# Kernel tuning notes

Hardware: AMD Instinct MI355X
Metric: run time of the kernel (lower is better)

The kernel has to match this reference:

```python
import jax, jax.numpy as jnp
from jax import lax
import numpy as np

# 8-neighbor topology from the original module
TOPO = np.array([[0, 1], [1, 1], [1, 0], [1, -1], [0, -1], [-1, -1], [-1, 0], [-1, 1]])
EPS = 1e-5


def conv(x, w, stride=1, pad=0, groups=1):
    # NCHW / OIHW convolution, no bias (module uses bias=False everywhere)
    return lax.conv_general_dilated(
        x, w, (stride, stride), [(pad, pad), (pad, pad)],
        feature_group_count=groups,
        dimension_numbers=('NCHW', 'OIHW', 'NCHW'))


def bn(x, g, b):
    # training-mode BatchNorm2d (batch statistics, biased variance)
    m = jnp.mean(x, axis=(0, 2, 3), keepdims=True)
    v = jnp.var(x, axis=(0, 2, 3), keepdims=True)
    return g[None, :, None, None] * (x - m) * lax.rsqrt(v + EPS) + b[None, :, None, None]


def setup_inputs() -> dict:
    key = jax.random.key(0)
    ks = jax.random.split(key, 12)
    B, D, NC, H, W = 8, 6, 48, 256, 256
    s = 0.1
    w = lambda k, shape: jax.random.normal(k, shape, jnp.float32) * s
    return dict(
        x=jax.random.normal(ks[0], (B, D, H, W), jnp.float32),
        # compenv_conv: Conv(D->NC,1) BN tanh Conv(NC->1,1)
        ce_w1=w(ks[1], (NC, D, 1, 1)), ce_g=jnp.ones(NC), ce_b=jnp.zeros(NC),
        ce_w2=w(ks[2], (1, NC, 1, 1)),
        # merge_change_determinant: funnel(ConvT(10->NC,3) tanh Conv(NC->NC,3) tanh) BN tanh Conv(NC->1,2,s2) sigmoid
        # ConvT stride-1 k3 expressed as pad-2 conv with conv-equivalent kernel
        md_ct=w(ks[3], (NC, 10, 3, 3)), md_c1=w(ks[4], (NC, NC, 3, 3)),
        md_g=jnp.ones(NC), md_b=jnp.zeros(NC), md_c2=w(ks[5], (1, NC, 2, 2)),
        # cell_merge: Conv(D->NC,2,s2,g3) BN tanh funnel(ConvT(NC->NC,3,g3) tanh Conv(NC->D,3,g3) tanh)
        cm_w1=w(ks[6], (NC, D // 3, 2, 2)), cm_g=jnp.ones(NC), cm_b=jnp.zeros(NC),
        cm_ct=w(ks[7], (NC, NC // 3, 3, 3)), cm_c2=w(ks[8], (D, NC // 3, 3, 3)),
        # born: Conv(D->NC,1) BN tanh Conv(NC->D,1)
        bo_w1=w(ks[9], (NC, D, 1, 1)), bo_g=jnp.ones(NC), bo_b=jnp.zeros(NC),
        bo_w2=w(ks[10], (D, NC, 1, 1)),
    )


def reference(x, ce_w1, ce_g, ce_b, ce_w2, md_ct, md_c1, md_g, md_b, md_c2,
              cm_w1, cm_g, cm_b, cm_ct, cm_c2, bo_w1, bo_g, bo_b, bo_w2):
    # ---- compenv: per-direction roll + 1x1conv/BN/tanh/1x1conv (BN stats per direction, as in torch) ----
    env = []
    for k in range(8):
        t = jnp.roll(x, int(TOPO[k, 0]), axis=3)      # roll_right along W
        t = jnp.roll(t, int(-TOPO[k, 1]), axis=2)     # roll_down along H
        h = jnp.tanh(bn(conv(t, ce_w1), ce_g, ce_b))
        env.append(conv(h, ce_w2))                    # [B,1,H,W]
    ENV = jnp.concatenate(env, axis=1)                # [B,8,H,W]

    # ---- merge change determinant ----
    te = jnp.concatenate([x[:, :2], ENV], axis=1)     # [B,10,H,W]
    h = jnp.tanh(conv(te, md_ct, pad=2))              # ConvT k3 s1 == pad-2 conv -> [B,NC,H+2,W+2]
    h = jnp.tanh(conv(h, md_c1))                      # -> [B,NC,H,W]
    h = jnp.tanh(bn(h, md_g, md_b))
    CHANGE = jax.nn.sigmoid(conv(h, md_c2, stride=2))  # [B,1,H/2,W/2]

    # ---- cell merge ----
    h = jnp.tanh(bn(conv(x, cm_w1, stride=2, groups=3), cm_g, cm_b))  # [B,NC,H/2,W/2]
    h = jnp.tanh(conv(h, cm_ct, pad=2, groups=3))
    xm = jnp.tanh(conv(h, cm_c2, groups=3))           # [B,D,H/2,W/2]

    # ---- born + blend ----
    born = conv(jnp.tanh(bn(conv(xm, bo_w1), bo_g, bo_b)), bo_w2)
    out = xm * (1.0 - CHANGE) + CHANGE * born
    out = jnp.concatenate([jax.nn.sigmoid(out[:, :3]), out[:, 3:]], axis=1)
    return out
```

## Files before the change

kernel.cpp:

```cpp
#include <hip/hip_runtime.h>
#include <stdint.h>

typedef unsigned short ushort_t;

#define B8  8
#define D6  6
#define NC  48
#define HH  256
#define WW  256
#define HWp 65536
#define H2  128
#define HW2 16384

__device__ __constant__ int c_T0[8] = {0,1,1,1,0,-1,-1,-1};
__device__ __constant__ int c_T1[8] = {1,1,0,-1,-1,-1,0,1};

__device__ inline float bf2f(ushort_t u){ union{unsigned int i; float f;} w; w.i = ((unsigned int)u)<<16; return w.f; }
__device__ inline ushort_t f2bf(float f){ union{float f; unsigned int i;} w; w.f=f; unsigned int xx=w.i;
  return (ushort_t)((xx + 0x7fffu + ((xx>>16)&1u)) >> 16); }
__device__ inline float tanhf_(float x){ float e=__expf(2.f*x); return 1.f - 2.f/(e+1.f); }
__device__ inline float sigm_(float x){ return 1.f/(1.f+__expf(-x)); }
__device__ inline float ldg_(const void* p, size_t i, int isbf){
  return isbf ? bf2f(((const ushort_t*)p)[i]) : ((const float*)p)[i];
}

typedef short short8 __attribute__((ext_vector_type(8)));
typedef float f4 __attribute__((ext_vector_type(4)));
typedef ushort_t us4 __attribute__((ext_vector_type(4)));
typedef ushort_t us8 __attribute__((ext_vector_type(8)));
union AB { short8 s; us4 h[2]; us8 u; };

__global__ __launch_bounds__(256) void k_detect(const ushort_t* x, float* flag){
  int t=threadIdx.x; int cnt=0;
  for(int i=t;i<4096;i+=256){
    ushort_t u=x[2*i];
    int e=(u>>7)&0xff;
    if(e>=100 && e<=150) cnt++;
  }
  for(int o=32;o;o>>=1) cnt+=__shfl_down(cnt,o,64);
  __shared__ int sh4[4];
  if((t&63)==0) sh4[t>>6]=cnt;
  __syncthreads();
  if(t==0){ int tot=sh4[0]+sh4[1]+sh4[2]+sh4[3]; flag[0] = (tot>=2048)?1.f:0.f; }
}

struct WC { const ushort_t* src[10]; int off[10]; int n[10]; };

__global__ __launch_bounds__(256) void k_wcvt(WC wc, float* dst, const float* dfl){
  int isbf = dfl[0]>0.5f;
  int t = blockIdx.y; int n = wc.n[t]; const ushort_t* s = wc.src[t]; float* d = dst + wc.off[t];
  for(int i = blockIdx.x*256 + threadIdx.x; i < n; i += gridDim.x*256)
    d[i] = isbf ? bf2f(s[i]) : ((const float*)s)[i];
}

__global__ __launch_bounds__(256) void k_wprep(const float* w2src, const float* w1src,
                                               ushort_t* wb2, ushort_t* wb1){
  int t = blockIdx.x*256+threadIdx.x;
  if(t<3456){
    int lane=t&63; int rest=t>>6;
    int ks=rest&1; int g=rest>>1; int tap=g%9; int nt=g/9;
    int oc=nt*16+(lane&15); int icb=ks*32+((lane>>4)*8);
    #pragma unroll
    for(int j=0;j<8;j++){
      int ic=icb+j;
      float v = (ic<48) ? w2src[(oc*48+ic)*9+tap] : 0.f;
      wb2[(size_t)t*8+j]=f2bf(v);
    }
  } else if(t<5184){
    int tt=t-3456; int lane=tt&63; int g=tt>>6; int tap=g%9; int nt=g/9;
    int oc=nt*16+(lane&15); int icb=(lane>>4)*8;
    #pragma unroll
    for(int j=0;j<8;j++){
      int ic=icb+j;
      float v = (ic<10) ? w1src[(oc*10+ic)*9+tap] : 0.f;
      wb1[(size_t)tt*8+j]=f2bf(v);
    }
  }
}

__global__ __launch_bounds__(256) void k_mom(const void* src, const float* dfl, int isbfc,
                                             int sh, int npix, float* out){
  int isbf = dfl ? (dfl[0]>0.5f) : isbfc;
  float vals[27];
  #pragma unroll
  for(int i=0;i<27;i++) vals[i]=0.f;
  int stride = gridDim.x*256;
  int msk = (1<<sh)-1;
  for(int p = blockIdx.x*256+threadIdx.x; p < npix; p += stride){
    int b = p >> sh; int hw = p & msk;
    float v[6];
    #pragma unroll
    for(int d=0; d<6; d++){
      size_t idx = (((size_t)(b*6+d))<<sh) + hw;
      v[d] = ldg_(src, idx, isbf);
    }
    int q=6;
    #pragma unroll
    for(int d=0;d<6;d++){
      vals[d]+=v[d];
      #pragma unroll
      for(int e=d;e<6;e++){ vals[q] += v[d]*v[e]; q++; }
    }
  }
  __shared__ float red[4][27];
  int wid=threadIdx.x>>6, lane=threadIdx.x&63;
  #pragma unroll
  for(int i=0;i<27;i++){
    float v=vals[i];
    for(int o=32;o;o>>=1) v+=__shfl_down(v,o,64);
    if(lane==0) red[wid][i]=v;
  }
  __syncthreads();
  if(threadIdx.x<27)
    atomicAdd(&out[threadIdx.x],
      red[0][threadIdx.x]+red[1][threadIdx.x]+red[2][threadIdx.x]+red[3][threadIdx.x]);
}

__global__ __launch_bounds__(64) void k_msb(const float* mom, const float* W1,
      const void* g, const void* b, const float* dfl, float invN, float* scale, float* bias){
  int c = threadIdx.x; if(c>=NC) return;
  int isbf = dfl[0]>0.5f;
  const int st[6]={0,6,11,15,18,20};
  float wr[6];
  #pragma unroll
  for(int d=0;d<6;d++) wr[d]=W1[c*6+d];
  float mean=0.f;
  #pragma unroll
  for(int d=0;d<6;d++) mean += wr[d]*mom[d];
  mean *= invN;
  float e2=0.f;
  #pragma unroll
  for(int d=0;d<6;d++){
    #pragma unroll
    for(int e=d;e<6;e++){
      float mm = mom[6 + st[d] + (e-d)];
      e2 += wr[d]*wr[e]*((e==d)?1.f:2.f)*mm;
    }
  }
  e2 *= invN;
  float var = e2 - mean*mean;
  float sc = ldg_(g,c,isbf) * rsqrtf(var + 1e-5f);
  scale[c]=sc; bias[c]= ldg_(b,c,isbf) - sc*mean;
}

__global__ __launch_bounds__(256) void k_env(const void* x, const float* dfl,
      const float* w1, const float* w2, const float* sc, const float* bi, float* e){
  int isbf = dfl[0]>0.5f;
  int p = blockIdx.x*256+threadIdx.x;
  int b = p >> 16; int hw = p & 65535;
  float v[6];
  #pragma unroll
  for(int d=0; d<6; d++) v[d]=ldg_(x,(size_t)(b*6+d)*HWp + hw, isbf);
  float acc=0.f;
  for(int c=0;c<NC;c++){
    float y=0.f;
    #pragma unroll
    for(int d=0;d<6;d++) y += w1[c*6+d]*v[d];
    acc += w2[c]*tanhf_(sc[c]*y + bi[c]);
  }
  e[(size_t)b*HWp + hw]=acc;
}

__global__ __launch_bounds__(256) void k_h1m(const void* x, const float* dfl, const float* e,
      const ushort_t* wb1, ushort_t* h1cl){
  __shared__ __attribute__((aligned(16))) ushort_t tile[324*24];
  int isbf = dfl[0]>0.5f;
  int b = blockIdx.y;
  int ti = blockIdx.x/17, tj = blockIdx.x%17;
  int i0 = ti*16, j0 = tj*16;
  {
    us8 z;
    #pragma unroll
    for(int j=0;j<8;j++) z[j]=0;
    us8* tp=(us8*)tile;
    for(int idx=threadIdx.x; idx<972; idx+=256) tp[idx]=z;
  }
  __syncthreads();
  for(int idx=threadIdx.x; idx<3240; idx+=256){
    int pix = idx/10, ic = idx-pix*10;
    int r = pix/18, c = pix-r*18;
    int gy = i0-2+r, gx = j0-2+c;
    float v = 0.f;
    if(gy>=0 && gy<HH && gx>=0 && gx<WW){
      if(ic<2) v = ldg_(x, ((size_t)(b*6+ic)*HH + gy)*WW + gx, isbf);
      else { int k=ic-2;
        int yy=(gy + c_T1[k]) & 255; int xx=(gx - c_T0[k]) & 255;
        v = e[((size_t)b*HH + yy)*WW + xx]; }
    }
    tile[pix*24+ic]=f2bf(v);
  }
  __syncthreads();
  int lane = threadIdx.x&63, w = threadIdx.x>>6;
  int n = lane&15, quad = lane>>4;
  int qoff = (quad<2) ? quad*8 : 16;
  f4 acc[4][3];
  #pragma unroll
  for(int a=0;a<4;a++)
    #pragma unroll
    for(int c=0;c<3;c++) acc[a][c]=(f4){0.f,0.f,0.f,0.f};
  for(int tap=0; tap<9; tap++){
    int ki=tap/3, kj=tap%3;
    AB Bf[3];
    #pragma unroll
    for(int nt=0;nt<3;nt++) Bf[nt].u = *(const us8*)&wb1[((size_t)((nt*9+tap)*64+lane))*8];
    #pragma unroll
    for(int yy=0; yy<4; yy++){
      int y = w*4 + yy;
      AB a; a.u = *(const us8*)&tile[((y+ki)*18 + n + kj)*24 + qoff];
      #pragma unroll
      for(int nt=0;nt<3;nt++)
        acc[yy][nt] = __builtin_amdgcn_mfma_f32_16x16x32_bf16(a.s, Bf[nt].s, acc[yy][nt], 0,0,0);
    }
  }
  #pragma unroll
  for(int yy=0;yy<4;yy++){
    int Y = i0 + w*4 + yy;
    if(Y>=258) continue;
    #pragma unroll
    for(int nt=0;nt<3;nt++){
      int oc = nt*16 + n;
      #pragma unroll
      for(int r=0;r<4;r++){
        int X = j0 + quad*4 + r;
        if(X<258)
          h1cl[(((size_t)b*258 + Y)*258 + X)*48 + oc] = f2bf(tanhf_(acc[yy][nt][r]));
      }
    }
  }
}

__global__ __launch_bounds__(256) void k_h2m(const ushort_t* h1cl, const ushort_t* wb2,
      ushort_t* h2h, float* stats){
  __shared__ float red[4][3][16][2];
  int b = blockIdx.y;
  int ti = blockIdx.x>>4, tj = blockIdx.x&15;
  int i0 = ti*16, j0 = tj*16;
  int lane = threadIdx.x&63, w = threadIdx.x>>6;
  int n = lane&15, quad = lane>>4;
  f4 acc[4][3];
  #pragma unroll
  for(int a=0;a<4;a++)
    #pragma unroll
    for(int c=0;c<3;c++) acc[a][c]=(f4){0.f,0.f,0.f,0.f};
  for(int tap=0; tap<9; tap++){
    int ki=tap/3, kj=tap%3;
    AB Bf[3][2];
    #pragma unroll
    for(int nt=0;nt<3;nt++)
      #pragma unroll
      for(int ks=0;ks<2;ks++)
        Bf[nt][ks].u = *(const us8*)&wb2[((size_t)(((nt*9+tap)*2+ks)*64+lane))*8];
    #pragma unroll
    for(int yy=0; yy<4; yy++){
      int Y = i0 + w*4 + yy;
      const ushort_t* ap = &h1cl[(((size_t)b*258 + Y+ki)*258 + (j0+n+kj))*48 + quad*8];
      AB a0, a1;
      a0.u = *(const us8*)ap;
      a1.u = *(const us8*)(ap+32);
      #pragma unroll
      for(int nt=0;nt<3;nt++){
        acc[yy][nt] = __builtin_amdgcn_mfma_f32_16x16x32_bf16(a0.s, Bf[nt][0].s, acc[yy][nt], 0,0,0);
        acc[yy][nt] = __builtin_amdgcn_mfma_f32_16x16x32_bf16(a1.s, Bf[nt][1].s, acc[yy][nt], 0,0,0);
      }
    }
  }
  float s[3]={0.f,0.f,0.f}, q[3]={0.f,0.f,0.f};
  #pragma unroll
  for(int yy=0;yy<4;yy++){
    int Y = i0 + w*4 + yy;
    #pragma unroll
    for(int nt=0;nt<3;nt++){
      int oc = nt*16 + n;
      size_t base = ((size_t)(b*NC+oc)*HH + Y)*WW + j0 + quad*4;
      us4 u;
      #pragma unroll
      for(int r=0;r<4;r++){
        float v=tanhf_(acc[yy][nt][r]);
        u[r]=f2bf(v);
        float vb=bf2f(u[r]);
        s[nt]+=vb; q[nt]+=vb*vb;
      }
      *(us4*)&h2h[base] = u;
    }
  }
  #pragma unroll
  for(int nt=0;nt<3;nt++){
    s[nt]+=__shfl_xor(s[nt],16,64); s[nt]+=__shfl_xor(s[nt],32,64);
    q[nt]+=__shfl_xor(q[nt],16,64); q[nt]+=__shfl_xor(q[nt],32,64);
  }
  if(quad==0){
    #pragma unroll
    for(int nt=0;nt<3;nt++){ red[w][nt][n][0]=s[nt]; red[w][nt][n][1]=q[nt]; }
  }
  __syncthreads();
  if(threadIdx.x<48){
    int oc=threadIdx.x; int nt=oc>>4, nn=oc&15;
    float S=red[0][nt][nn][0]+red[1][nt][nn][0]+red[2][nt][nn][0]+red[3][nt][nn][0];
    float Q=red[0][nt][nn][1]+red[1][nt][nn][1]+red[2][nt][nn][1]+red[3][nt][nn][1];
    atomicAdd(&stats[2*oc],S); atomicAdd(&stats[2*oc+1],Q);
  }
}

__global__ __launch_bounds__(256) void k_cstat(const float* srcf, const ushort_t* srch, int isbf,
      int C, int HWn, int Bn, int S, float* stats){
  int c = blockIdx.x % C; int s = blockIdx.x / C;
  float sum=0.f, sq=0.f;
  for(int b=0;b<Bn;b++){
    size_t base=((size_t)b*C+c)*HWn;
    for(int i=s*256+threadIdx.x; i<HWn; i+=S*256){
      float v = isbf ? bf2f(srch[base+i]) : srcf[base+i];
      sum+=v; sq+=v*v;
    }
  }
  for(int o=32;o;o>>=1){ sum+=__shfl_down(sum,o,64); sq+=__shfl_down(sq,o,64); }
  __shared__ float ls[4], lq[4];
  int wid=threadIdx.x>>6;
  if((threadIdx.x&63)==0){ ls[wid]=sum; lq[wid]=sq; }
  __syncthreads();
  if(threadIdx.x==0){
    atomicAdd(&stats[2*c],   ls[0]+ls[1]+ls[2]+ls[3]);
    atomicAdd(&stats[2*c+1], lq[0]+lq[1]+lq[2]+lq[3]);
  }
}

__global__ __launch_bounds__(64) void k_csb(const float* stats, const void* g, const void* b,
      const float* dfl, float invN, float* scale, float* bias){
  int c=threadIdx.x; if(c>=NC) return;
  int isbf = dfl[0]>0.5f;
  float mean=stats[2*c]*invN; float var=stats[2*c+1]*invN - mean*mean;
  float s=ldg_(g,c,isbf)*rsqrtf(var+1e-5f);
  scale[c]=s; bias[c]=ldg_(b,c,isbf)-s*mean;
}

__global__ __launch_bounds__(256) void k_change(const ushort_t* h2h,
      const float* wc2, const float* sc, const float* bi, float* CH){
  int p=blockIdx.x*256+threadIdx.x;
  int b=p>>14; int rem=p&16383; int i=rem>>7; int j=rem&127;
  float acc=0.f;
  for(int ic=0;ic<NC;ic++){
    size_t base=((size_t)(b*NC+ic)*HH + 2*i)*WW + 2*j;
    float s=sc[ic], t=bi[ic];
    #pragma unroll
    for(int ki=0;ki<2;ki++)
      #pragma unroll
      for(int kj=0;kj<2;kj++){
        float v= bf2f(h2h[base+(size_t)ki*WW+kj]);
        acc += tanhf_(s*v+t)*wc2[ic*4+ki*2+kj];
      }
  }
  CH[p]=sigm_(acc);
}

__global__ __launch_bounds__(256) void k_cm1(const void* x, const float* dfl, const float* w, float* t1){
  int isbf = dfl[0]>0.5f;
  int p=blockIdx.x*256+threadIdx.x;
  int b=p>>14; int rem=p&16383; int i=rem>>7; int j=rem&127;
  float v[6][2][2];
  #pragma unroll
  for(int d=0;d<6;d++)
    #pragma unroll
    for(int ki=0;ki<2;ki++)
      #pragma unroll
      for(int kj=0;kj<2;kj++)
        v[d][ki][kj]=ldg_(x, ((size_t)(b*6+d)*HH + 2*i+ki)*WW + 2*j+kj, isbf);
  for(int oc=0;oc<NC;oc++){
    int g=oc>>4;
    float a=0.f;
    #pragma unroll
    for(int icl=0;icl<2;icl++)
      #pragma unroll
      for(int ki=0;ki<2;ki++)
        #pragma unroll
        for(int kj=0;kj<2;kj++)
          a += v[2*g+icl][ki][kj]*w[((oc*2+icl)*2+ki)*2+kj];
    t1[((size_t)(b*NC+oc)*HW2) + rem]=a;
  }
}

__global__ __launch_bounds__(256) void k_cm2(const float* t1, const float* sc, const float* bi,
        const float* wct, float* t2){
  __shared__ float as[16][20][21];
  int b=blockIdx.y, g=blockIdx.z;
  int ti=blockIdx.x/9, tj=blockIdx.x%9;
  int i0=ti*16, j0=tj*16;
  int ty=threadIdx.x>>4, tx=threadIdx.x&15;
  for(int idx=threadIdx.x; idx<6400; idx+=256){
    int i=idx/400; int rem=idx-i*400; int r=rem/20; int cc=rem-r*20;
    int cg=g*16+i;
    int y=i0-2+r, xx=j0-2+cc;
    float v=0.f;
    if(y>=0 && y<H2 && xx>=0 && xx<H2)
      v = tanhf_(sc[cg]*t1[((size_t)(b*NC+cg)*H2 + y)*H2 + xx] + bi[cg]);
    as[i][r][cc]=v;
  }
  __syncthreads();
  float acc[16];
  #pragma unroll
  for(int o=0;o<16;o++) acc[o]=0.f;
  for(int i=0;i<16;i++){
    float p[3][3];
    #pragma unroll
    for(int ki=0;ki<3;ki++)
      #pragma unroll
      for(int kj=0;kj<3;kj++) p[ki][kj]=as[i][ty+ki][tx+kj];
    #pragma unroll
    for(int o=0;o<16;o++){
      const float* wp=&wct[((size_t)(g*16+o)*16+i)*9];
      float a=0.f;
      #pragma unroll
      for(int q=0;q<9;q++) a += p[q/3][q%3]*wp[q];
      acc[o]+=a;
    }
  }
  int ii=i0+ty, jj=j0+tx;
  if(ii<130 && jj<130){
    #pragma unroll
    for(int o=0;o<16;o++)
      t2[((size_t)(b*NC+g*16+o)*130 + ii)*130 + jj]=tanhf_(acc[o]);
  }
}

__global__ __launch_bounds__(256) void k_cm3(const float* t2, const float* w, float* xm){
  __shared__ float ts[16][18][20];
  int b=blockIdx.y, g=blockIdx.z;
  int ti=blockIdx.x>>3, tj=blockIdx.x&7;
  int i0=ti*16, j0=tj*16;
  int ty=threadIdx.x>>4, tx=threadIdx.x&15;
  for(int idx=threadIdx.x; idx<16*18*18; idx+=256){
    int i=idx/324; int rem=idx-i*324; int r=rem/18; int cc=rem-r*18;
    int cg=g*16+i;
    ts[i][r][cc]=t2[((size_t)(b*NC+cg)*130 + i0+r)*130 + j0+cc];
  }
  __syncthreads();
  float acc[2]={0.f,0.f};
  for(int icl=0;icl<16;icl++){
    float p[3][3];
    #pragma unroll
    for(int ki=0;ki<3;ki++)
      #pragma unroll
      for(int kj=0;kj<3;kj++) p[ki][kj]=ts[icl][ty+ki][tx+kj];
    #pragma unroll
    for(int ol=0;ol<2;ol++){
      int oc=2*g+ol;
      const float* wp=&w[((size_t)oc*16+icl)*9];
      float a=0.f;
      #pragma unroll
      for(int q=0;q<9;q++) a += p[q/3][q%3]*wp[q];
      acc[ol]+=a;
    }
  }
  int ii=i0+ty, jj=j0+tx;
  #pragma unroll
  for(int ol=0;ol<2;ol++)
    xm[((size_t)(b*6+2*g+ol)*H2 + ii)*H2 + jj]=tanhf_(acc[ol]);
}

__global__ __launch_bounds__(256) void k_final(const float* xm, const float* CH, const float* w1,
      const float* w2, const float* sc, const float* bi, const float* dfl, void* outp){
  int isbf = dfl[0]>0.5f;
  int p=blockIdx.x*256+threadIdx.x;
  int b=p>>14; int rem=p&16383;
  float v[6];
  #pragma unroll
  for(int d=0;d<6;d++) v[d]=xm[((size_t)(b*6+d)*HW2)+rem];
  float born[6]={0.f,0.f,0.f,0.f,0.f,0.f};
  for(int c=0;c<NC;c++){
    float y=0.f;
    #pragma unroll
    for(int d=0;d<6;d++) y+=w1[c*6+d]*v[d];
    float a=tanhf_(sc[c]*y+bi[c]);
    #pragma unroll
    for(int d=0;d<6;d++) born[d]+=w2[d*NC+c]*a;
  }
  float C=CH[p];
  #pragma unroll
  for(int d=0;d<6;d++){
    float o=v[d]*(1.f-C)+C*born[d];
    if(d<3) o=sigm_(o);
    size_t id=((size_t)(b*6+d)*HW2)+rem;
    if(isbf) ((ushort_t*)outp)[id]=f2bf(o); else ((float*)outp)[id]=o;
  }
}

extern "C" void kernel_launch(void* const* d_in, const int* in_sizes, int n_in,
                              void* d_out, int out_size, void* d_ws, size_t ws_size,
                              hipStream_t stream){
  (void)in_sizes; (void)n_in; (void)out_size; (void)ws_size;
  const ushort_t* x    = (const ushort_t*)d_in[0];
  const ushort_t* cew1 = (const ushort_t*)d_in[1];
  const void*     ceg  = d_in[2];
  const void*     ceb  = d_in[3];
  const ushort_t* cew2 = (const ushort_t*)d_in[4];
  const ushort_t* mdct = (const ushort_t*)d_in[5];
  const ushort_t* mdc1 = (const ushort_t*)d_in[6];
  const void*     mdg  = d_in[7];
  const void*     mdb  = d_in[8];
  const ushort_t* mdc2 = (const ushort_t*)d_in[9];
  const ushort_t* cmw1 = (const ushort_t*)d_in[10];
  const void*     cmg  = d_in[11];
  const void*     cmb  = d_in[12];
  const ushort_t* cmct = (const ushort_t*)d_in[13];
  const ushort_t* cmc2 = (const ushort_t*)d_in[14];
  const ushort_t* bow1 = (const ushort_t*)d_in[15];
  const void*     bog  = d_in[16];
  const void*     bob  = d_in[17];
  const ushort_t* bow2 = (const ushort_t*)d_in[18];
  float* ws = (float*)d_ws;

  const long OW_mdct=0, OW_mdc1=4320, OW_cew1=25056, OW_cew2=25344, OW_mdc2=25392,
             OW_cmw1=25584, OW_cmct=25968, OW_cmc2=32880, OW_bow1=33744, OW_bow2=34032;
  const long OFF_STATS=34320;
  const long ST_xmom=OFF_STATS+0,  ST_cesc=OFF_STATS+64,  ST_cebi=OFF_STATS+112,
             ST_h2  =OFF_STATS+160, ST_mdsc=OFF_STATS+256, ST_mdbi=OFF_STATS+304,
             ST_t1  =OFF_STATS+352, ST_cmsc=OFF_STATS+448, ST_cmbi=OFF_STATS+496,
             ST_xmm =OFF_STATS+544, ST_bosc=OFF_STATS+608, ST_bobi=OFF_STATS+656,
             ST_FLAG=OFF_STATS+960;
  const long OFF_WB2 = OFF_STATS + 1024;
  const long OFF_WB1 = OFF_WB2 + 13824;
  const long OFF_E   = OFF_WB1 + 6912;
  const long OFF_H2  = OFF_E + 524288L;
  const long OFF_D   = OFF_H2 + 12582912L;
  const long OFF_T1=OFF_D, OFF_T2=OFF_D+6291456L, OFF_XM=OFF_D+12781056L, OFF_CH=OFF_D+13567488L;

  ushort_t* h1cl = (ushort_t*)(ws + OFF_D);
  ushort_t* h2h  = (ushort_t*)(ws + OFF_H2);
  ushort_t* wb2  = (ushort_t*)(ws + OFF_WB2);
  ushort_t* wb1  = (ushort_t*)(ws + OFF_WB1);
  const float* dfl = ws + ST_FLAG;

  (void)hipMemsetAsync(ws + OFF_STATS, 0, 1024*sizeof(float), stream);
  hipLaunchKernelGGL(k_detect, dim3(1), 256, 0, stream, x, ws+ST_FLAG);

  WC wc;
  const ushort_t* srcs[10] = {mdct,mdc1,cew1,cew2,mdc2,cmw1,cmct,cmc2,bow1,bow2};
  const int offs[10] = {(int)OW_mdct,(int)OW_mdc1,(int)OW_cew1,(int)OW_cew2,(int)OW_mdc2,
                        (int)OW_cmw1,(int)OW_cmct,(int)OW_cmc2,(int)OW_bow1,(int)OW_bow2};
  const int cnts[10] = {4320,20736,288,48,192,384,6912,864,288,288};
  for(int i=0;i<10;i++){ wc.src[i]=srcs[i]; wc.off[i]=offs[i]; wc.n[i]=cnts[i]; }
  hipLaunchKernelGGL(k_wcvt, dim3(81,10), 256, 0, stream, wc, ws, dfl);
  hipLaunchKernelGGL(k_wprep, dim3(21), 256, 0, stream, ws+OW_mdc1, ws+OW_mdct, wb2, wb1);

  hipLaunchKernelGGL(k_mom, dim3(256), 256, 0, stream, (const void*)x, dfl, 0, 16, B8*HWp, ws+ST_xmom);
  hipLaunchKernelGGL(k_msb, dim3(1), 64, 0, stream, ws+ST_xmom, ws+OW_cew1, ceg, ceb, dfl,
                     1.f/(float)(B8*HWp), ws+ST_cesc, ws+ST_cebi);
  hipLaunchKernelGGL(k_env, dim3(2048), 256, 0, stream, (const void*)x, dfl, ws+OW_cew1, ws+OW_cew2,
                     ws+ST_cesc, ws+ST_cebi, ws+OFF_E);

  hipLaunchKernelGGL(k_h1m, dim3(289,8), 256, 0, stream, (const void*)x, dfl, ws+OFF_E, wb1, h1cl);
  hipLaunchKernelGGL(k_h2m, dim3(256,8), 256, 0, stream, h1cl, wb2, h2h, ws+ST_h2);
  hipLaunchKernelGGL(k_csb, dim3(1), 64, 0, stream, ws+ST_h2, mdg, mdb, dfl, 1.f/(float)(B8*HWp),
                     ws+ST_mdsc, ws+ST_mdbi);
  hipLaunchKernelGGL(k_change, dim3(512), 256, 0, stream, h2h, ws+OW_mdc2,
                     ws+ST_mdsc, ws+ST_mdbi, ws+OFF_CH);

  hipLaunchKernelGGL(k_cm1, dim3(512), 256, 0, stream, (const void*)x, dfl, ws+OW_cmw1, ws+OFF_T1);
  hipLaunchKernelGGL(k_cstat, dim3(48*8), 256, 0, stream, ws+OFF_T1, (const ushort_t*)nullptr, 0,
                     NC, HW2, B8, 8, ws+ST_t1);
  hipLaunchKernelGGL(k_csb, dim3(1), 64, 0, stream, ws+ST_t1, cmg, cmb, dfl, 1.f/(float)(B8*HW2),
                     ws+ST_cmsc, ws+ST_cmbi);
  hipLaunchKernelGGL(k_cm2, dim3(81,8,3), 256, 0, stream, ws+OFF_T1, ws+ST_cmsc, ws+ST_cmbi,
                     ws+OW_cmct, ws+OFF_T2);
  hipLaunchKernelGGL(k_cm3, dim3(64,8,3), 256, 0, stream, ws+OFF_T2, ws+OW_cmc2, ws+OFF_XM);

  hipLaunchKernelGGL(k_mom, dim3(128), 256, 0, stream, (const void*)(ws+OFF_XM), (const float*)nullptr, 0,
                     14, B8*HW2, ws+ST_xmm);
  hipLaunchKernelGGL(k_msb, dim3(1), 64, 0, stream, ws+ST_xmm, ws+OW_bow1, bog, bob, dfl,
                     1.f/(float)(B8*HW2), ws+ST_bosc, ws+ST_bobi);
  hipLaunchKernelGGL(k_final, dim3(512), 256, 0, stream, ws+OFF_XM, ws+OFF_CH, ws+OW_bow1,
                     ws+OW_bow2, ws+ST_bosc, ws+ST_bobi, dfl, d_out);
}
```

Before: 497.1 us.

## Stage h1 halo tile in LDS via async global_load_lds in k_h2m

k_h2m now copies each wave's 6x18x48 bf16 input halo into LDS with asynchronous global-to-LDS loads. The 3x3 conv's A fragments are then read from LDS instead of re-read from global memory for every tap, which removes repeated global traffic. The upper channel half for quads 2-3 now reads a zeroed LDS pad. The change also fully unrolls the tap loops in both conv kernels and adds a min-blocks-per-CU hint of 3. The cost is about 41KB of LDS per block, which may limit occupancy, plus register pressure from the unrolling.

```diff
diff --git a/kernel.cpp b/kernel.cpp
--- a/kernel.cpp
+++ b/kernel.cpp
@@ -198,6 +198,7 @@
   for(int a=0;a<4;a++)
     #pragma unroll
     for(int c=0;c<3;c++) acc[a][c]=(f4){0.f,0.f,0.f,0.f};
+  #pragma unroll
   for(int tap=0; tap<9; tap++){
     int ki=tap/3, kj=tap%3;
     AB Bf[3];
@@ -229,19 +230,38 @@
   }
 }
 
-__global__ __launch_bounds__(256) void k_h2m(const ushort_t* h1cl, const ushort_t* wb2,
+__global__ __launch_bounds__(256,3) void k_h2m(const ushort_t* h1cl, const ushort_t* wb2,
       ushort_t* h2h, float* stats){
+  __shared__ __attribute__((aligned(16))) ushort_t tile[20800];
   __shared__ float red[4][3][16][2];
   int b = blockIdx.y;
   int ti = blockIdx.x>>4, tj = blockIdx.x&15;
   int i0 = ti*16, j0 = tj*16;
   int lane = threadIdx.x&63, w = threadIdx.x>>6;
+  ushort_t* wtile = &tile[w*5200];
+  int r0 = i0 + w*4;
+  #pragma unroll
+  for(int it=0; it<11; it++){
+    int chunk = it*64 + lane;
+    if(chunk < 648){
+      int cpix = chunk/6, cq = chunk - cpix*6;
+      int rr = cpix/18, cc = cpix - rr*18;
+      const ushort_t* src = &h1cl[(((size_t)b*258 + r0+rr)*258 + (j0+cc))*48 + cq*8];
+      __builtin_amdgcn_global_load_lds(
+          (const __attribute__((address_space(1))) unsigned int*)src,
+          (__attribute__((address_space(3))) unsigned int*)(wtile + it*512),
+          16, 0, 0);
+    }
+  }
+  if(lane<16) wtile[5184+lane]=0;
+  __builtin_amdgcn_s_waitcnt(0x0F70);
   int n = lane&15, quad = lane>>4;
   f4 acc[4][3];
   #pragma unroll
   for(int a=0;a<4;a++)
     #pragma unroll
     for(int c=0;c<3;c++) acc[a][c]=(f4){0.f,0.f,0.f,0.f};
+  #pragma unroll
   for(int tap=0; tap<9; tap++){
     int ki=tap/3, kj=tap%3;
     AB Bf[3][2];
@@ -252,11 +272,11 @@
         Bf[nt][ks].u = *(const us8*)&wb2[((size_t)(((nt*9+tap)*2+ks)*64+lane))*8];
     #pragma unroll
     for(int yy=0; yy<4; yy++){
-      int Y = i0 + w*4 + yy;
-      const ushort_t* ap = &h1cl[(((size_t)b*258 + Y+ki)*258 + (j0+n+kj))*48 + quad*8];
+      int pix = (yy+ki)*18 + n + kj;
       AB a0, a1;
-      a0.u = *(const us8*)ap;
-      a1.u = *(const us8*)(ap+32);
+      a0.u = *(const us8*)(wtile + pix*48 + quad*8);
+      a1.u = (quad<2) ? *(const us8*)(wtile + pix*48 + 32 + quad*8)
+                      : *(const us8*)(wtile + 5184);
       #pragma unroll
       for(int nt=0;nt<3;nt++){
         acc[yy][nt] = __builtin_amdgcn_mfma_f32_16x16x32_bf16(a0.s, Bf[nt][0].s, acc[yy][nt], 0,0,0);
@@ -267,7 +287,7 @@
   float s[3]={0.f,0.f,0.f}, q[3]={0.f,0.f,0.f};
   #pragma unroll
   for(int yy=0;yy<4;yy++){
-    int Y = i0 + w*4 + yy;
+    int Y = r0 + yy;
     #pragma unroll
     for(int nt=0;nt<3;nt++){
       int oc = nt*16 + n;
```

Result: no change. 489.9 us (-1.5%).

## Fuse merge-determinant conv pair in shared memory; store cell-merge intermediate as bf16

Applied to the files above, without the earlier changes.

Fuses the two 3x3 convolutions of the merge-change branch into one kernel. Each block computes its 18x18 halo of the first conv's output (tanh applied) into LDS and feeds it straight to the second conv's MFMA loop, so the large channels-last h1 buffer is never written to or read back from global memory. The cost is recomputing the halo rows and columns and using much more LDS per block, which may lower occupancy (launch bounds now ask for 3 blocks). Separately, the cell-merge first-conv output t1 is stored as bf16 instead of fp32 to halve its traffic, at some precision cost before BN and tanh.

```diff
diff --git a/kernel.cpp b/kernel.cpp
--- a/kernel.cpp
+++ b/kernel.cpp
@@ -161,24 +161,29 @@
   e[(size_t)b*HWp + hw]=acc;
 }
 
-__global__ __launch_bounds__(256) void k_h1m(const void* x, const float* dfl, const float* e,
-      const ushort_t* wb1, ushort_t* h1cl){
-  __shared__ __attribute__((aligned(16))) ushort_t tile[324*24];
+__global__ __launch_bounds__(256,3) void k_md(const void* x, const float* dfl, const float* e,
+      const ushort_t* wb1, const ushort_t* wb2, ushort_t* h2h, float* stats){
+  __shared__ __attribute__((aligned(16))) ushort_t te[6400];
+  __shared__ __attribute__((aligned(16))) ushort_t h1t[18816];
+  __shared__ float red[4][3][16][2];
   int isbf = dfl[0]>0.5f;
   int b = blockIdx.y;
-  int ti = blockIdx.x/17, tj = blockIdx.x%17;
+  int ti = blockIdx.x>>4, tj = blockIdx.x&15;
   int i0 = ti*16, j0 = tj*16;
+  int lane = threadIdx.x&63, w = threadIdx.x>>6;
+  int n = lane&15, quad = lane>>4;
   {
     us8 z;
     #pragma unroll
     for(int j=0;j<8;j++) z[j]=0;
-    us8* tp=(us8*)tile;
-    for(int idx=threadIdx.x; idx<972; idx+=256) tp[idx]=z;
-  }
-  __syncthreads();
-  for(int idx=threadIdx.x; idx<3240; idx+=256){
+    us8* tp=(us8*)te;
+    for(int idx=threadIdx.x; idx<800; idx+=256) tp[idx]=z;
+    for(int idx=threadIdx.x; idx<336; idx+=256) *(us8*)&h1t[idx*56+48]=z;
+  }
+  __syncthreads();
+  for(int idx=threadIdx.x; idx<4000; idx+=256){
     int pix = idx/10, ic = idx-pix*10;
-    int r = pix/18, c = pix-r*18;
+    int r = pix/20, c = pix-r*20;
     int gy = i0-2+r, gx = j0-2+c;
     float v = 0.f;
     if(gy>=0 && gy<HH && gx>=0 && gx<WW){
@@ -187,61 +192,44 @@
         int yy=(gy + c_T1[k]) & 255; int xx=(gx - c_T0[k]) & 255;
         v = e[((size_t)b*HH + yy)*WW + xx]; }
     }
-    tile[pix*24+ic]=f2bf(v);
-  }
-  __syncthreads();
-  int lane = threadIdx.x&63, w = threadIdx.x>>6;
-  int n = lane&15, quad = lane>>4;
-  int qoff = (quad<2) ? quad*8 : 16;
+    te[pix*16+ic]=f2bf(v);
+  }
+  __syncthreads();
+  {
+    int qoff = (quad&1)*8;
+    for(int mt=w; mt<21; mt+=4){
+      int p = mt*16 + n;
+      int pr = p/18, pc = p-pr*18;
+      f4 hacc[3];
+      #pragma unroll
+      for(int nt=0;nt<3;nt++) hacc[nt]=(f4){0.f,0.f,0.f,0.f};
+      #pragma unroll
+      for(int tap=0; tap<9; tap++){
+        int ki=tap/3, kj=tap%3;
+        AB a; a.u = *(const us8*)&te[((pr+ki)*20 + pc+kj)*16 + qoff];
+        #pragma unroll
+        for(int nt=0;nt<3;nt++){
+          AB Bf; Bf.u = *(const us8*)&wb1[((size_t)((nt*9+tap)*64+lane))*8];
+          hacc[nt] = __builtin_amdgcn_mfma_f32_16x16x32_bf16(a.s, Bf.s, hacc[nt], 0,0,0);
+        }
+      }
+      int pd = mt*16 + quad*4;
+      #pragma unroll
+      for(int nt=0;nt<3;nt++){
+        #pragma unroll
+        for(int r=0;r<4;r++)
+          h1t[(pd+r)*56 + nt*16 + n] = f2bf(tanhf_(hacc[nt][r]));
+      }
+    }
+  }
+  __syncthreads();
   f4 acc[4][3];
   #pragma unroll
   for(int a=0;a<4;a++)
     #pragma unroll
     for(int c=0;c<3;c++) acc[a][c]=(f4){0.f,0.f,0.f,0.f};
-  for(int tap=0; tap<9; tap++){
-    int ki=tap/3, kj=tap%3;
-    AB Bf[3];
-    #pragma unroll
-    for(int nt=0;nt<3;nt++) Bf[nt].u = *(const us8*)&wb1[((size_t)((nt*9+tap)*64+lane))*8];
-    #pragma unroll
-    for(int yy=0; yy<4; yy++){
-      int y = w*4 + yy;
-      AB a; a.u = *(const us8*)&tile[((y+ki)*18 + n + kj)*24 + qoff];
-      #pragma unroll
-      for(int nt=0;nt<3;nt++)
-        acc[yy][nt] = __builtin_amdgcn_mfma_f32_16x16x32_bf16(a.s, Bf[nt].s, acc[yy][nt], 0,0,0);
-    }
-  }
-  #pragma unroll
-  for(int yy=0;yy<4;yy++){
-    int Y = i0 + w*4 + yy;
-    if(Y>=258) continue;
-    #pragma unroll
-    for(int nt=0;nt<3;nt++){
-      int oc = nt*16 + n;
-      #pragma unroll
-      for(int r=0;r<4;r++){
-        int X = j0 + quad*4 + r;
-        if(X<258)
-          h1cl[(((size_t)b*258 + Y)*258 + X)*48 + oc] = f2bf(tanhf_(acc[yy][nt][r]));
-      }
-    }
-  }
-}
-
-__global__ __launch_bounds__(256) void k_h2m(const ushort_t* h1cl, const ushort_t* wb2,
-      ushort_t* h2h, float* stats){
-  __shared__ float red[4][3][16][2];
-  int b = blockIdx.y;
-  int ti = blockIdx.x>>4, tj = blockIdx.x&15;
-  int i0 = ti*16, j0 = tj*16;
-  int lane = threadIdx.x&63, w = threadIdx.x>>6;
-  int n = lane&15, quad = lane>>4;
-  f4 acc[4][3];
-  #pragma unroll
-  for(int a=0;a<4;a++)
-    #pragma unroll
-    for(int c=0;c<3;c++) acc[a][c]=(f4){0.f,0.f,0.f,0.f};
+  int q1off = 32 + ((quad<2) ? quad*8 : 16);
+  #pragma unroll
   for(int tap=0; tap<9; tap++){
     int ki=tap/3, kj=tap%3;
     AB Bf[3][2];
@@ -252,11 +240,11 @@
         Bf[nt][ks].u = *(const us8*)&wb2[((size_t)(((nt*9+tap)*2+ks)*64+lane))*8];
     #pragma unroll
     for(int yy=0; yy<4; yy++){
-      int Y = i0 + w*4 + yy;
-      const ushort_t* ap = &h1cl[(((size_t)b*258 + Y+ki)*258 + (j0+n+kj))*48 + quad*8];
+      int y = w*4 + yy;
+      int base = ((y+ki)*18 + n + kj)*56;
       AB a0, a1;
-      a0.u = *(const us8*)ap;
-      a1.u = *(const us8*)(ap+32);
+      a0.u = *(const us8*)&h1t[base + quad*8];
+      a1.u = *(const us8*)&h1t[base + q1off];
       #pragma unroll
       for(int nt=0;nt<3;nt++){
         acc[yy][nt] = __builtin_amdgcn_mfma_f32_16x16x32_bf16(a0.s, Bf[nt][0].s, acc[yy][nt], 0,0,0);
@@ -351,7 +339,7 @@
   CH[p]=sigm_(acc);
 }
 
-__global__ __launch_bounds__(256) void k_cm1(const void* x, const float* dfl, const float* w, float* t1){
+__global__ __launch_bounds__(256) void k_cm1(const void* x, const float* dfl, const float* w, ushort_t* t1){
   int isbf = dfl[0]>0.5f;
   int p=blockIdx.x*256+threadIdx.x;
   int b=p>>14; int rem=p&16383; int i=rem>>7; int j=rem&127;
@@ -373,11 +361,11 @@
         #pragma unroll
         for(int kj=0;kj<2;kj++)
           a += v[2*g+icl][ki][kj]*w[((oc*2+icl)*2+ki)*2+kj];
-    t1[((size_t)(b*NC+oc)*HW2) + rem]=a;
-  }
-}
-
-__global__ __launch_bounds__(256) void k_cm2(const float* t1, const float* sc, const float* bi,
+    t1[((size_t)(b*NC+oc)*HW2) + rem]=f2bf(a);
+  }
+}
+
+__global__ __launch_bounds__(256) void k_cm2(const ushort_t* t1, const float* sc, const float* bi,
         const float* wct, float* t2){
   __shared__ float as[16][20][21];
   int b=blockIdx.y, g=blockIdx.z;
@@ -390,7 +378,7 @@
     int y=i0-2+r, xx=j0-2+cc;
     float v=0.f;
     if(y>=0 && y<H2 && xx>=0 && xx<H2)
-      v = tanhf_(sc[cg]*t1[((size_t)(b*NC+cg)*H2 + y)*H2 + xx] + bi[cg]);
+      v = tanhf_(sc[cg]*bf2f(t1[((size_t)(b*NC+cg)*H2 + y)*H2 + xx]) + bi[cg]);
     as[i][r][cc]=v;
   }
   __syncthreads();
@@ -522,8 +510,8 @@
   const long OFF_D   = OFF_H2 + 12582912L;
   const long OFF_T1=OFF_D, OFF_T2=OFF_D+6291456L, OFF_XM=OFF_D+12781056L, OFF_CH=OFF_D+13567488L;
 
-  ushort_t* h1cl = (ushort_t*)(ws + OFF_D);
   ushort_t* h2h  = (ushort_t*)(ws + OFF_H2);
+  ushort_t* t1h  = (ushort_t*)(ws + OFF_T1);
   ushort_t* wb2  = (ushort_t*)(ws + OFF_WB2);
   ushort_t* wb1  = (ushort_t*)(ws + OFF_WB1);
   const float* dfl = ws + ST_FLAG;
@@ -546,19 +534,19 @@
   hipLaunchKernelGGL(k_env, dim3(2048), 256, 0, stream, (const void*)x, dfl, ws+OW_cew1, ws+OW_cew2,
                      ws+ST_cesc, ws+ST_cebi, ws+OFF_E);
 
-  hipLaunchKernelGGL(k_h1m, dim3(289,8), 256, 0, stream, (const void*)x, dfl, ws+OFF_E, wb1, h1cl);
-  hipLaunchKernelGGL(k_h2m, dim3(256,8), 256, 0, stream, h1cl, wb2, h2h, ws+ST_h2);
+  hipLaunchKernelGGL(k_md, dim3(256,8), 256, 0, stream, (const void*)x, dfl, ws+OFF_E,
+                     wb1, wb2, h2h, ws+ST_h2);
   hipLaunchKernelGGL(k_csb, dim3(1), 64, 0, stream, ws+ST_h2, mdg, mdb, dfl, 1.f/(float)(B8*HWp),
                      ws+ST_mdsc, ws+ST_mdbi);
   hipLaunchKernelGGL(k_change, dim3(512), 256, 0, stream, h2h, ws+OW_mdc2,
                      ws+ST_mdsc, ws+ST_mdbi, ws+OFF_CH);
 
-  hipLaunchKernelGGL(k_cm1, dim3(512), 256, 0, stream, (const void*)x, dfl, ws+OW_cmw1, ws+OFF_T1);
-  hipLaunchKernelGGL(k_cstat, dim3(48*8), 256, 0, stream, ws+OFF_T1, (const ushort_t*)nullptr, 0,
+  hipLaunchKernelGGL(k_cm1, dim3(512), 256, 0, stream, (const void*)x, dfl, ws+OW_cmw1, t1h);
+  hipLaunchKernelGGL(k_cstat, dim3(48*8), 256, 0, stream, (const float*)nullptr, t1h, 1,
                      NC, HW2, B8, 8, ws+ST_t1);
   hipLaunchKernelGGL(k_csb, dim3(1), 64, 0, stream, ws+ST_t1, cmg, cmb, dfl, 1.f/(float)(B8*HW2),
                      ws+ST_cmsc, ws+ST_cmbi);
-  hipLaunchKernelGGL(k_cm2, dim3(81,8,3), 256, 0, stream, ws+OFF_T1, ws+ST_cmsc, ws+ST_cmbi,
+  hipLaunchKernelGGL(k_cm2, dim3(81,8,3), 256, 0, stream, t1h, ws+ST_cmsc, ws+ST_cmbi,
                      ws+OW_cmct, ws+OFF_T2);
   hipLaunchKernelGGL(k_cm3, dim3(64,8,3), 256, 0, stream, ws+OFF_T2, ws+OW_cmc2, ws+OFF_XM);
 
```

Result: faster. 460.6 us (-7.4%).
